# Kernel tuning notes

Measured on AMD Instinct MI355X. Metric: run time of the kernel, lower is better.

Reference implementation:

```python
import jax, jax.numpy as jnp
import numpy as np

B, C, Hf, Wf = 32, 512, 16, 16
S = Hf * Wf            # 256 kv tokens
D = 2048               # d_model
DIN = 512              # d_input (attention embed dim)
HEADS = 8
DH = DIN // HEADS
T = 50                 # iterations (internal ticks)
M = 25                 # memory_length
HH = 16                # memory_hidden_dims
NSA = 512              # n_synch_action
NSO = 512              # n_synch_out
OUT = 1000             # out_dims


def _ln(x, g, b, eps=1e-5):
    mu = x.mean(-1, keepdims=True)
    var = ((x - mu) ** 2).mean(-1, keepdims=True)
    return (x - mu) / jnp.sqrt(var + eps) * g + b


def _glu(x):
    a, b = jnp.split(x, 2, axis=-1)
    return a * jax.nn.sigmoid(b)


def setup_inputs() -> dict:
    key = jax.random.key(0)
    ki = iter(jax.random.split(key, 40))
    def rn(shape, s=0.02):
        return jax.random.normal(next(ki), shape, jnp.float32) * s
    inp = {}
    inp['x'] = jax.random.normal(next(ki), (B, C, Hf, Wf), jnp.float32)
    # kv_proj: Linear(C->DIN) + LayerNorm
    inp['kv_w'] = rn((C, DIN)); inp['kv_b'] = jnp.zeros((DIN,), jnp.float32)
    inp['ln_kv_g'] = jnp.ones((DIN,), jnp.float32); inp['ln_kv_b'] = jnp.zeros((DIN,), jnp.float32)
    # q_proj: Linear(NSA->DIN)
    inp['q_w'] = rn((NSA, DIN)); inp['q_b'] = jnp.zeros((DIN,), jnp.float32)
    # MultiheadAttention projections
    inp['Wq'] = rn((DIN, DIN)); inp['bq'] = jnp.zeros((DIN,), jnp.float32)
    inp['Wk'] = rn((DIN, DIN)); inp['bk'] = jnp.zeros((DIN,), jnp.float32)
    inp['Wv'] = rn((DIN, DIN)); inp['bv'] = jnp.zeros((DIN,), jnp.float32)
    inp['Wo'] = rn((DIN, DIN)); inp['bo'] = jnp.zeros((DIN,), jnp.float32)
    # synapse: Linear(DIN+D -> 2D) + GLU + LayerNorm(D)
    inp['syn_w'] = rn((DIN + D, 2 * D)); inp['syn_b'] = jnp.zeros((2 * D,), jnp.float32)
    inp['ln_syn_g'] = jnp.ones((D,), jnp.float32); inp['ln_syn_b'] = jnp.zeros((D,), jnp.float32)
    # per-neuron NLMs (SuperLinear weights: (in,out,N))
    inp['nlm_w1'] = rn((M, 2 * HH, D), 0.1); inp['nlm_b1'] = jnp.zeros((1, D, 2 * HH), jnp.float32)
    inp['nlm_w2'] = rn((HH, 2, D), 0.1); inp['nlm_b2'] = jnp.zeros((1, D, 2), jnp.float32)
    # output projector
    inp['out_w'] = rn((NSO, OUT)); inp['out_b'] = jnp.zeros((OUT,), jnp.float32)
    # learnable decay params (clamped to [0,15] in forward)
    inp['decay_action'] = jax.random.uniform(next(ki), (NSA,), jnp.float32)
    inp['decay_out'] = jax.random.uniform(next(ki), (NSO,), jnp.float32)
    # learned start state
    inp['start_trace'] = rn((D, M), 0.05)
    inp['start_act'] = rn((D,), 0.05)
    # random-pairing neuron indices (fixed at init in the original)
    inp['idx_la'] = jax.random.randint(next(ki), (NSA,), 0, D)
    inp['idx_ra'] = jax.random.randint(next(ki), (NSA,), 0, D)
    inp['idx_lo'] = jax.random.randint(next(ki), (NSO,), 0, D)
    inp['idx_ro'] = jax.random.randint(next(ki), (NSO,), 0, D)
    return inp


def reference(x, kv_w, kv_b, ln_kv_g, ln_kv_b, q_w, q_b, Wq, bq, Wk, bk, Wv, bv, Wo, bo,
              syn_w, syn_b, ln_syn_g, ln_syn_b, nlm_w1, nlm_b1, nlm_w2, nlm_b2,
              out_w, out_b, decay_action, decay_out, start_trace, start_act,
              idx_la, idx_ra, idx_lo, idx_ro):
    # featurise: identity backbone, flatten spatial to tokens, project to DIN
    feats = x.reshape(B, C, S).transpose(0, 2, 1)                 # (B,S,C)
    kv = _ln(feats @ kv_w + kv_b, ln_kv_g, ln_kv_b)               # (B,S,DIN)
    kh = (kv @ Wk + bk).reshape(B, S, HEADS, DH).transpose(0, 2, 1, 3)  # (B,H,S,DH)
    vh = (kv @ Wv + bv).reshape(B, S, HEADS, DH).transpose(0, 2, 1, 3)
    r_a = jnp.exp(-jnp.clip(decay_action, 0.0, 15.0))[None]       # (1,NSA)
    r_o = jnp.exp(-jnp.clip(decay_out, 0.0, 15.0))[None]          # (1,NSO)

    def nlm(trace):  # per-neuron MLP over the memory axis: (B,D,M) -> (B,D)
        h = _glu(jnp.einsum('bdm,mhd->bdh', trace, nlm_w1) + nlm_b1)
        return _glu(jnp.einsum('bdh,hod->bdo', h, nlm_w2) + nlm_b2)[..., 0]

    act0 = jnp.broadcast_to(start_act[None], (B, D))
    trace0 = jnp.broadcast_to(start_trace[None], (B, D, M))
    # out-synchronisation initialised from the start state (before the loop)
    a_o0 = act0[:, idx_lo] * act0[:, idx_ro]
    b_o0 = jnp.ones_like(a_o0)
    a_a0 = jnp.zeros((B, NSA), jnp.float32)
    b_a0 = jnp.zeros((B, NSA), jnp.float32)
    log_out = jnp.log(jnp.float32(OUT))
    scale = 1.0 / jnp.sqrt(jnp.float32(DH))

    def step(carry, _):
        trace, act, a_a, b_a, a_o, b_o = carry
        # action synchronisation (decayed pairwise products, sync = alpha/sqrt(beta))
        a_a = r_a * a_a + act[:, idx_la] * act[:, idx_ra]
        b_a = r_a * b_a + 1.0
        sync_a = a_a / jnp.sqrt(b_a)
        # attention readout (single query token)
        q = sync_a @ q_w + q_b                                    # (B,DIN)
        qh = (q @ Wq + bq).reshape(B, HEADS, 1, DH)
        attn = jax.nn.softmax(jnp.einsum('bhqd,bhkd->bhqk', qh, kh) * scale, -1)
        o = jnp.einsum('bhqk,bhkd->bhqd', attn, vh).transpose(0, 2, 1, 3).reshape(B, DIN)
        attn_out = o @ Wo + bo
        # synapse MLP -> new pre-activation state
        pre = jnp.concatenate([attn_out, act], axis=-1)           # (B,DIN+D)
        state = _ln(_glu(pre @ syn_w + syn_b), ln_syn_g, ln_syn_b)
        trace = jnp.concatenate([trace[:, :, 1:], state[:, :, None]], axis=-1)
        act = nlm(trace)                                          # (B,D)
        # output synchronisation + prediction
        a_o = r_o * a_o + act[:, idx_lo] * act[:, idx_ro]
        b_o = r_o * b_o + 1.0
        sync_o = a_o / jnp.sqrt(b_o)
        pred = sync_o @ out_w + out_b                             # (B,OUT)
        logp = jax.nn.log_softmax(pred, -1)
        ne = -(jnp.exp(logp) * logp).sum(-1) / log_out
        cert = jnp.stack([ne, 1.0 - ne], axis=-1)                 # (B,2)
        return (trace, act, a_a, b_a, a_o, b_o), (pred, cert, sync_o)

    _, (preds, certs, syncs) = jax.lax.scan(step, (trace0, act0, a_a0, b_a0, a_o0, b_o0), None, length=T)
    predictions = jnp.transpose(preds, (1, 2, 0))                 # (B,OUT,T)
    certainties = jnp.transpose(certs, (1, 2, 0))                 # (B,2,T)
    return predictions, certainties, syncs[-1]
```

## Files before the change

### kernel.cpp

```cpp
#include <hip/hip_runtime.h>
#include <math.h>

#define BB 32
#define CC 512
#define SS 256
#define DD 2048
#define DIN 512
#define NH 8
#define DHD 64
#define TT 50
#define MM 25
#define HHID 16
#define NSA 512
#define NSO 512
#define NOUT 1000

__global__ void init_kernel(const float* __restrict__ dec_a, const float* __restrict__ dec_o,
                            const float* __restrict__ start_act, const float* __restrict__ start_trace,
                            const int* __restrict__ idx_lo, const int* __restrict__ idx_ro,
                            float* __restrict__ r_a, float* __restrict__ r_o,
                            float* __restrict__ a_a, float* __restrict__ b_a,
                            float* __restrict__ a_o, float* __restrict__ b_o,
                            float* __restrict__ trace)
{
    int i = blockIdx.x * 256 + threadIdx.x;
    if (i < 512) {
        r_a[i] = expf(-fminf(fmaxf(dec_a[i], 0.f), 15.f));
        r_o[i] = expf(-fminf(fmaxf(dec_o[i], 0.f), 15.f));
    }
    if (i < BB * NSA) {
        a_a[i] = 0.f; b_a[i] = 0.f;
        int j = i & 511;
        a_o[i] = start_act[idx_lo[j]] * start_act[idx_ro[j]];
        b_o[i] = 1.f;
    }
    if (i < BB * MM * DD) {
        int rem = i % (MM * DD);
        int m = rem / DD, d = rem % DD;
        trace[i] = start_trace[d * MM + m];
    }
}

template<int AMODE, int SMODE>
__global__ void gemm64(const float* __restrict__ A, const float* __restrict__ Bm,
                       const float* __restrict__ bias, float* __restrict__ Cm,
                       int Mdim, int Ndim, int Kdim)
{
    __shared__ float As[16 * 65];
    __shared__ float Bs[16 * 64];
    int row0 = blockIdx.x * 64;
    int col0 = blockIdx.y * 64;
    int t = threadIdx.x;
    int tx = t & 15, ty = t >> 4;
    float acc[4][4] = {};
    for (int k0 = 0; k0 < Kdim; k0 += 16) {
        if (AMODE == 0) {
            for (int i = t; i < 1024; i += 256) {
                int kk = i & 15, r = i >> 4;
                As[kk * 65 + r] = A[(size_t)(row0 + r) * Kdim + k0 + kk];
            }
        } else {
            int b = row0 / SS, s0 = row0 % SS;
            for (int i = t; i < 1024; i += 256) {
                int r = i & 63, kk = i >> 6;
                As[kk * 65 + r] = A[((size_t)b * CC + k0 + kk) * SS + s0 + r];
            }
        }
        for (int i = t; i < 1024; i += 256) {
            int c = i & 63, kk = i >> 6;
            Bs[kk * 64 + c] = Bm[(size_t)(k0 + kk) * Ndim + col0 + c];
        }
        __syncthreads();
        #pragma unroll
        for (int kk = 0; kk < 16; ++kk) {
            float a[4], bb[4];
            #pragma unroll
            for (int i = 0; i < 4; i++) a[i] = As[kk * 65 + ty * 4 + i];
            #pragma unroll
            for (int j = 0; j < 4; j++) bb[j] = Bs[kk * 64 + tx * 4 + j];
            #pragma unroll
            for (int i = 0; i < 4; i++)
                #pragma unroll
                for (int j = 0; j < 4; j++) acc[i][j] += a[i] * bb[j];
        }
        __syncthreads();
    }
    #pragma unroll
    for (int i = 0; i < 4; i++)
        #pragma unroll
        for (int j = 0; j < 4; j++) {
            int row = row0 + ty * 4 + i, col = col0 + tx * 4 + j;
            float v = acc[i][j] + (bias ? bias[col] : 0.f);
            if (SMODE == 0) {
                Cm[(size_t)row * Ndim + col] = v;
            } else if (SMODE == 1) {
                int b = row / SS, s = row % SS, h = col >> 6, dh = col & 63;
                Cm[(((size_t)b * NH + h) * DHD + dh) * SS + s] = v;
            } else {
                int b = row / SS, s = row % SS, h = col >> 6, dh = col & 63;
                Cm[(((size_t)b * NH + h) * SS + s) * DHD + dh] = v;
            }
        }
}

__global__ void ln_rows(float* __restrict__ buf, const float* __restrict__ g,
                        const float* __restrict__ bta)
{
    int row = blockIdx.x, t = threadIdx.x;
    __shared__ float red[256];
    float v0 = buf[(size_t)row * 512 + t];
    float v1 = buf[(size_t)row * 512 + 256 + t];
    red[t] = v0 + v1; __syncthreads();
    for (int off = 128; off; off >>= 1) { if (t < off) red[t] += red[t + off]; __syncthreads(); }
    float mu = red[0] * (1.f / 512.f); __syncthreads();
    float d0 = v0 - mu, d1 = v1 - mu;
    red[t] = d0 * d0 + d1 * d1; __syncthreads();
    for (int off = 128; off; off >>= 1) { if (t < off) red[t] += red[t + off]; __syncthreads(); }
    float rstd = 1.f / sqrtf(red[0] * (1.f / 512.f) + 1e-5f);
    buf[(size_t)row * 512 + t]       = d0 * rstd * g[t] + bta[t];
    buf[(size_t)row * 512 + 256 + t] = d1 * rstd * g[t + 256] + bta[t + 256];
}

__global__ void bqq_kernel(const float* __restrict__ q_b, const float* __restrict__ Wq,
                           const float* __restrict__ bq, float* __restrict__ bqq)
{
    int c = blockIdx.x * 256 + threadIdx.x;
    if (c >= 512) return;
    float acc = bq[c];
    for (int k = 0; k < 512; k++) acc += q_b[k] * Wq[k * 512 + c];
    bqq[c] = acc;
}

__global__ void bias2_kernel(const float* __restrict__ bo, const float* __restrict__ syn_w,
                             const float* __restrict__ syn_b, float* __restrict__ bias2)
{
    int c = blockIdx.x * 256 + threadIdx.x;
    if (c >= 4096) return;
    float acc = syn_b[c];
    for (int k = 0; k < 512; k++) acc += bo[k] * syn_w[(size_t)k * 4096 + c];
    bias2[c] = acc;
}

__global__ void pad_act0(const float* __restrict__ out_w, const float* __restrict__ out_b,
                         const float* __restrict__ start_act,
                         float* __restrict__ out_wp, float* __restrict__ out_bp,
                         float* __restrict__ act0slot)
{
    int i = blockIdx.x * 256 + threadIdx.x;
    if (i < 512 * 1024) {
        int r = i >> 10, c = i & 1023;
        out_wp[i] = (c < 1000) ? out_w[r * 1000 + c] : 0.f;
    }
    if (i < 1024) out_bp[i] = (i < 1000) ? out_b[i] : 0.f;
    if (i < BB * DD) act0slot[i] = start_act[i & (DD - 1)];
}

__global__ __launch_bounds__(256) void k1_front(
    const float* __restrict__ act, const int* __restrict__ la, const int* __restrict__ ra,
    const float* __restrict__ r_a,
    const float* __restrict__ aold, const float* __restrict__ bold,
    float* __restrict__ anew, float* __restrict__ bnew,
    const float* __restrict__ Wqq, const float* __restrict__ bqq,
    const float* __restrict__ khT, const float* __restrict__ vh,
    float* __restrict__ obuf)
{
    __shared__ float sa[512];
    __shared__ float qp[256];
    __shared__ float qs[64];
    __shared__ float ps[256];
    __shared__ float red[256];
    int bh = blockIdx.x, b = bh >> 3, h = bh & 7;
    int tid = threadIdx.x;
    const float* actb = act + b * DD;
    for (int j = tid; j < 512; j += 256) {
        float p = actb[la[j]] * actb[ra[j]];
        float r = r_a[j];
        float aa = r * aold[b * 512 + j] + p;
        float bb = r * bold[b * 512 + j] + 1.f;
        sa[j] = aa / sqrtf(bb);
        if (h == 0) { anew[b * 512 + j] = aa; bnew[b * 512 + j] = bb; }
    }
    __syncthreads();
    {
        int cl = tid & 63, q = tid >> 6;
        const float* wcol = Wqq + h * 64 + cl;
        float acc = 0.f;
        #pragma unroll 8
        for (int k = q * 128; k < q * 128 + 128; ++k)
            acc += sa[k] * wcol[k * 512];
        qp[tid] = acc;
    }
    __syncthreads();
    if (tid < 64)
        qs[tid] = qp[tid] + qp[tid + 64] + qp[tid + 128] + qp[tid + 192] + bqq[h * 64 + tid];
    __syncthreads();
    const float* kb = khT + (size_t)bh * 64 * 256;
    float sc = 0.f;
    #pragma unroll 8
    for (int dh = 0; dh < 64; ++dh) sc += qs[dh] * kb[dh * 256 + tid];
    sc *= 0.125f;
    red[tid] = sc; __syncthreads();
    for (int off = 128; off; off >>= 1) { if (tid < off) red[tid] = fmaxf(red[tid], red[tid + off]); __syncthreads(); }
    float mx = red[0]; __syncthreads();
    float e = expf(sc - mx);
    red[tid] = e; __syncthreads();
    for (int off = 128; off; off >>= 1) { if (tid < off) red[tid] += red[tid + off]; __syncthreads(); }
    float inv = 1.f / red[0];
    ps[tid] = e * inv;
    __syncthreads();
    int dh = tid & 63, ch = tid >> 6;
    const float* vb = vh + (size_t)bh * 256 * 64;
    float acc = 0.f;
    for (int s = ch * 64; s < ch * 64 + 64; ++s) acc += ps[s] * vb[s * 64 + dh];
    red[tid] = acc; __syncthreads();
    if (tid < 128) red[tid] += red[tid + 128];
    __syncthreads();
    if (tid < 64) obuf[b * 512 + h * 64 + tid] = red[tid] + red[tid + 64];
}

#define SYN_PAD 164
__global__ __launch_bounds__(256) void k2_syn(
    const float* __restrict__ obuf, const float* __restrict__ act,
    const float* __restrict__ W2, const float* __restrict__ syn_w,
    float* __restrict__ upart)
{
    __shared__ float As[32 * SYN_PAD];
    int tid = threadIdx.x;
    int ks = blockIdx.x & 3, ct = blockIdx.x >> 2;
    int cgr = tid & 7, r = tid >> 3;
    int c = ct * 32 + cgr * 4;
    int kbase0 = ks * 640;
    float acc0 = 0.f, acc1 = 0.f, acc2 = 0.f, acc3 = 0.f;
    for (int ri = 0; ri < 4; ++ri) {
        __syncthreads();
        #pragma unroll
        for (int q = 0; q < 5; ++q) {
            int i = tid + q * 256;
            int rr = i / 40, kg = i % 40;
            int k = kbase0 + ri * 160 + kg * 4;
            float4 v;
            if (k < 512) v = *(const float4*)(obuf + rr * 512 + k);
            else         v = *(const float4*)(act + rr * 2048 + (k - 512));
            *(float4*)(As + rr * SYN_PAD + kg * 4) = v;
        }
        __syncthreads();
        const float* Ar = As + r * SYN_PAD;
        int kbase = kbase0 + ri * 160;
        for (int kk = 0; kk < 160; kk += 8) {
            float4 wreg[8];
            #pragma unroll
            for (int u8 = 0; u8 < 8; ++u8) {
                int kg = kbase + kk + u8;
                const float* wr = (kg < 512 ? W2 : syn_w) + (size_t)kg * 4096 + c;
                wreg[u8] = *(const float4*)wr;
            }
            #pragma unroll
            for (int u8 = 0; u8 < 8; ++u8) {
                float a = Ar[kk + u8];
                acc0 += a * wreg[u8].x; acc1 += a * wreg[u8].y;
                acc2 += a * wreg[u8].z; acc3 += a * wreg[u8].w;
            }
        }
    }
    *(float4*)(upart + (size_t)ks * (32 * 4096) + r * 4096 + c) =
        make_float4(acc0, acc1, acc2, acc3);
}

__global__ __launch_bounds__(256) void k34_glunlm(
    const float* __restrict__ upart, const float* __restrict__ bias2,
    const float* __restrict__ g, const float* __restrict__ bta,
    float* __restrict__ trace,
    const float* __restrict__ w1, const float* __restrict__ b1,
    const float* __restrict__ w2, const float* __restrict__ b2,
    float* __restrict__ actout, int t_iter)
{
    __shared__ float red[256];
    int blk = blockIdx.x, tid = threadIdx.x;
    int b = blk >> 3, dtile = blk & 7;
    const float* u0 = upart + (size_t)b * 4096;
    float vals[8];
    float loc = 0.f;
    #pragma unroll
    for (int ii = 0; ii < 8; ++ii) {
        int d = tid + ii * 256;
        float a = bias2[d], bb = bias2[d + 2048];
        #pragma unroll
        for (int ks = 0; ks < 4; ++ks) {
            const float* up = u0 + (size_t)ks * (32 * 4096);
            a += up[d];
            bb += up[d + 2048];
        }
        float gl = a * (1.f / (1.f + expf(-bb)));
        vals[ii] = gl; loc += gl;
    }
    red[tid] = loc; __syncthreads();
    for (int off = 128; off; off >>= 1) { if (tid < off) red[tid] += red[tid + off]; __syncthreads(); }
    float mu = red[0] * (1.f / 2048.f); __syncthreads();
    float l2 = 0.f;
    #pragma unroll
    for (int ii = 0; ii < 8; ++ii) { float dq = vals[ii] - mu; l2 += dq * dq; }
    red[tid] = l2; __syncthreads();
    for (int off = 128; off; off >>= 1) { if (tid < off) red[tid] += red[tid + off]; __syncthreads(); }
    float rstd = 1.f / sqrtf(red[0] * (1.f / 2048.f) + 1e-5f);
    int d0 = dtile * 256 + tid;
    float a0 = bias2[d0], bb0 = bias2[d0 + 2048];
    #pragma unroll
    for (int ks = 0; ks < 4; ++ks) {
        const float* up = u0 + (size_t)ks * (32 * 4096);
        a0 += up[d0];
        bb0 += up[d0 + 2048];
    }
    float gl0 = a0 * (1.f / (1.f + expf(-bb0)));
    float nv = (gl0 - mu) * rstd * g[d0] + bta[d0];
    int newrow = t_iter % MM;
    trace[((size_t)b * MM + newrow) * DD + d0] = nv;
    float hp[32];
    #pragma unroll
    for (int h = 0; h < 32; h++) hp[h] = b1[d0 * 32 + h];
    const float* tr = trace + (size_t)b * MM * DD;
    for (int m = 0; m < 24; m++) {
        int mph = (t_iter + 1 + m) % 25;
        float tv = tr[mph * DD + d0];
        #pragma unroll
        for (int h = 0; h < 32; h++) hp[h] += tv * w1[((size_t)m * 32 + h) * DD + d0];
    }
    #pragma unroll
    for (int h = 0; h < 32; h++) hp[h] += nv * w1[((size_t)24 * 32 + h) * DD + d0];
    float o0 = b2[d0 * 2], o1 = b2[d0 * 2 + 1];
    #pragma unroll
    for (int h = 0; h < 16; h++) {
        float hv = hp[h] * (1.f / (1.f + expf(-hp[h + 16])));
        o0 += hv * w2[((size_t)h * 2) * DD + d0];
        o1 += hv * w2[((size_t)h * 2 + 1) * DD + d0];
    }
    actout[b * DD + d0] = o0 * (1.f / (1.f + expf(-o1)));
}

__global__ __launch_bounds__(256) void k_syncscan(
    const float* __restrict__ acthist, const int* __restrict__ lo, const int* __restrict__ ro,
    const float* __restrict__ r_o,
    const float* __restrict__ a_o0, const float* __restrict__ b_o0,
    float* __restrict__ so_hist, float* __restrict__ out_sync)
{
    int idx = blockIdx.x * 256 + threadIdx.x;
    int b = idx >> 9, j = idx & 511;
    float aa = a_o0[idx], bb = b_o0[idx];
    float rr = r_o[j];
    int il = lo[j], ir = ro[j];
    const float* ah = acthist + (size_t)(BB * DD) + b * DD;
    float s = 0.f;
    for (int t = 0; t < TT; ++t) {
        float p = ah[il] * ah[ir];
        aa = rr * aa + p;
        bb = rr * bb + 1.f;
        s = aa / sqrtf(bb);
        so_hist[(size_t)t * (BB * 512) + idx] = s;
        ah += BB * DD;
    }
    out_sync[idx] = s;
}

__global__ __launch_bounds__(256) void k6_cert(
    const float* __restrict__ predt, float* __restrict__ d_out)
{
    int t_iter = blockIdx.x >> 5, b = blockIdx.x & 31, t = threadIdx.x;
    __shared__ float red[256];
    const float* pr = predt + ((size_t)t_iter * 32 + b) * 1024;
    float pv[4];
    float mx = -1e30f;
    #pragma unroll
    for (int ii = 0; ii < 4; ++ii) {
        int c = t + ii * 256;
        float v = -1e30f;
        if (c < 1000) {
            v = pr[c];
            d_out[(size_t)b * NOUT * TT + (size_t)c * TT + t_iter] = v;
        }
        pv[ii] = v;
        mx = fmaxf(mx, v);
    }
    red[t] = mx; __syncthreads();
    for (int off = 128; off; off >>= 1) { if (t < off) red[t] = fmaxf(red[t], red[t + off]); __syncthreads(); }
    mx = red[0]; __syncthreads();
    float s1 = 0.f, s2 = 0.f;
    #pragma unroll
    for (int ii = 0; ii < 4; ++ii) {
        int c = t + ii * 256;
        if (c < 1000) { float xx = pv[ii] - mx; float e = expf(xx); s1 += e; s2 += e * xx; }
    }
    red[t] = s1; __syncthreads();
    for (int off = 128; off; off >>= 1) { if (t < off) red[t] += red[t + off]; __syncthreads(); }
    s1 = red[0]; __syncthreads();
    red[t] = s2; __syncthreads();
    for (int off = 128; off; off >>= 1) { if (t < off) red[t] += red[t + off]; __syncthreads(); }
    s2 = red[0];
    if (t == 0) {
        float ne = -(s2 / s1 - logf(s1)) * (1.f / logf(1000.f));
        size_t base = (size_t)BB * NOUT * TT + (size_t)b * 2 * TT + t_iter;
        d_out[base] = ne;
        d_out[base + TT] = 1.f - ne;
    }
}

extern "C" void kernel_launch(void* const* d_in, const int* in_sizes, int n_in,
                              void* d_out, int out_size, void* d_ws, size_t ws_size,
                              hipStream_t stream)
{
    const float* x        = (const float*)d_in[0];
    const float* kv_w     = (const float*)d_in[1];
    const float* kv_b     = (const float*)d_in[2];
    const float* ln_kv_g  = (const float*)d_in[3];
    const float* ln_kv_b  = (const float*)d_in[4];
    const float* q_w      = (const float*)d_in[5];
    const float* q_b      = (const float*)d_in[6];
    const float* Wq       = (const float*)d_in[7];
    const float* bq       = (const float*)d_in[8];
    const float* Wk       = (const float*)d_in[9];
    const float* bk       = (const float*)d_in[10];
    const float* Wv       = (const float*)d_in[11];
    const float* bv       = (const float*)d_in[12];
    const float* Wo       = (const float*)d_in[13];
    const float* bo       = (const float*)d_in[14];
    const float* syn_w    = (const float*)d_in[15];
    const float* syn_b    = (const float*)d_in[16];
    const float* ln_syn_g = (const float*)d_in[17];
    const float* ln_syn_b = (const float*)d_in[18];
    const float* nlm_w1   = (const float*)d_in[19];
    const float* nlm_b1   = (const float*)d_in[20];
    const float* nlm_w2   = (const float*)d_in[21];
    const float* nlm_b2   = (const float*)d_in[22];
    const float* out_w    = (const float*)d_in[23];
    const float* out_b    = (const float*)d_in[24];
    const float* dec_a    = (const float*)d_in[25];
    const float* dec_o    = (const float*)d_in[26];
    const float* start_tr = (const float*)d_in[27];
    const float* start_ac = (const float*)d_in[28];
    const int*   idx_la   = (const int*)d_in[29];
    const int*   idx_ra   = (const int*)d_in[30];
    const int*   idx_lo   = (const int*)d_in[31];
    const int*   idx_ro   = (const int*)d_in[32];
    float* out = (float*)d_out;

    float* w = (float*)d_ws;
    float* kvbuf = w;            w += (size_t)8192 * 512;
    float* khT   = w;            w += (size_t)8192 * 512;
    float* vhb   = w;            w += (size_t)8192 * 512;
    float* Wqq   = w;            w += (size_t)512 * 512;
    float* bqq   = w;            w += 512;
    float* W2    = w;            w += (size_t)512 * 4096;
    float* bias2 = w;            w += 4096;
    float* r_a   = w;            w += 512;
    float* r_o   = w;            w += 512;
    float* a_a   = w;            w += 2 * BB * NSA;
    float* b_a   = w;            w += 2 * BB * NSA;
    float* a_o   = w;            w += BB * NSO;
    float* b_o   = w;            w += BB * NSO;
    float* trace = w;            w += (size_t)BB * MM * DD;
    float* obuf  = w;            w += BB * DIN;
    float* upart = w;            w += (size_t)4 * 32 * 4096;
    float* so_hist = w;          w += (size_t)TT * BB * 512;
    float* predt = w;            w += (size_t)TT * BB * 1024;
    float* out_wp = w;           w += (size_t)512 * 1024;
    float* out_bp = w;           w += 1024;

    float* acthist = kvbuf;

    init_kernel<<<6400, 256, 0, stream>>>(dec_a, dec_o, start_ac, start_tr, idx_lo, idx_ro,
                                          r_a, r_o, a_a, b_a, a_o, b_o, trace);
    gemm64<1, 0><<<dim3(128, 8), 256, 0, stream>>>(x, kv_w, kv_b, kvbuf, 8192, 512, 512);
    ln_rows<<<8192, 256, 0, stream>>>(kvbuf, ln_kv_g, ln_kv_b);
    gemm64<0, 1><<<dim3(128, 8), 256, 0, stream>>>(kvbuf, Wk, bk, khT, 8192, 512, 512);
    gemm64<0, 2><<<dim3(128, 8), 256, 0, stream>>>(kvbuf, Wv, bv, vhb, 8192, 512, 512);
    gemm64<0, 0><<<dim3(8, 8), 256, 0, stream>>>(q_w, Wq, nullptr, Wqq, 512, 512, 512);
    bqq_kernel<<<2, 256, 0, stream>>>(q_b, Wq, bq, bqq);
    gemm64<0, 0><<<dim3(8, 64), 256, 0, stream>>>(Wo, syn_w, nullptr, W2, 512, 4096, 512);
    bias2_kernel<<<16, 256, 0, stream>>>(bo, syn_w, syn_b, bias2);
    pad_act0<<<2048, 256, 0, stream>>>(out_w, out_b, start_ac, out_wp, out_bp, acthist);

    float* out_sync = out + (size_t)BB * NOUT * TT + (size_t)BB * 2 * TT;

    for (int t = 0; t < TT; ++t) {
        int par = t & 1;
        const float* act_t = acthist + (size_t)t * (BB * DD);
        float* act_n = acthist + (size_t)(t + 1) * (BB * DD);
        k1_front<<<256, 256, 0, stream>>>(act_t, idx_la, idx_ra, r_a,
                                          a_a + par * (BB * 512), b_a + par * (BB * 512),
                                          a_a + (par ^ 1) * (BB * 512), b_a + (par ^ 1) * (BB * 512),
                                          Wqq, bqq, khT, vhb, obuf);
        k2_syn<<<512, 256, 0, stream>>>(obuf, act_t, W2, syn_w, upart);
        k34_glunlm<<<256, 256, 0, stream>>>(upart, bias2, ln_syn_g, ln_syn_b, trace,
                                            nlm_w1, nlm_b1, nlm_w2, nlm_b2, act_n, t);
    }

    k_syncscan<<<64, 256, 0, stream>>>(acthist, idx_lo, idx_ro, r_o, a_o, b_o,
                                       so_hist, out_sync);
    gemm64<0, 0><<<dim3(25, 16), 256, 0, stream>>>(so_hist, out_wp, out_bp, predt,
                                                   1600, 1024, 512);
    k6_cert<<<1600, 256, 0, stream>>>(predt, out);
}
```

Before: 5.209 ms.

## Fuse synapse GEMM with GLU and LN partial stats, stage NLM weights in LDS

Pre-transposes the combined synapse weight into a k-contiguous WT layout. The per-step synapse GEMM now computes both GLU halves per output column over the full K, with no split-K. The kernel applies GLU in place and emits per-batch sum and sum-of-squares partials, which removes the upart round trip and the LayerNorm re-reduction. The NLM kernel is retiled to 8 batches × 32 neurons and stages its w1 slice (about 100KB) in dynamic LDS. Variance is now computed as E[x^2]-mu^2, which is less numerically stable. The large LDS use limits occupancy, and each block in the GEMM kernel covers only 8 columns with per-thread strided weight reads.

Result: slower. 5.901 ms (+13.3%).

```diff
diff --git a/kernel.cpp b/kernel.cpp
--- a/kernel.cpp
+++ b/kernel.cpp
@@ -141,10 +141,36 @@
     bias2[c] = acc;
 }
 
-__global__ void pad_act0(const float* __restrict__ out_w, const float* __restrict__ out_b,
-                         const float* __restrict__ start_act,
-                         float* __restrict__ out_wp, float* __restrict__ out_bp,
-                         float* __restrict__ act0slot)
+__global__ void wt_build(const float* __restrict__ W2, const float* __restrict__ syn_w,
+                         float* __restrict__ WT)
+{
+    __shared__ float tile[32][33];
+    int k0 = blockIdx.x * 32, c0 = blockIdx.y * 32;
+    int t = threadIdx.x;
+    int col = t & 31, rq = t >> 5;
+    #pragma unroll
+    for (int q = 0; q < 4; ++q) {
+        int kk = q * 8 + rq;
+        int k = k0 + kk;
+        const float* src = (k < 512 ? W2 : syn_w) + (size_t)k * 4096 + c0;
+        tile[kk][col] = src[col];
+    }
+    __syncthreads();
+    #pragma unroll
+    for (int q = 0; q < 4; ++q) {
+        int cc = q * 8 + rq;
+        WT[(size_t)(c0 + cc) * 2560 + k0 + col] = tile[col][cc];
+    }
+}
+
+__global__ void act0_kernel(const float* __restrict__ start_act, float* __restrict__ act0slot)
+{
+    int i = blockIdx.x * 256 + threadIdx.x;
+    if (i < BB * DD) act0slot[i] = start_act[i & (DD - 1)];
+}
+
+__global__ void pad_outw(const float* __restrict__ out_w, const float* __restrict__ out_b,
+                         float* __restrict__ out_wp, float* __restrict__ out_bp)
 {
     int i = blockIdx.x * 256 + threadIdx.x;
     if (i < 512 * 1024) {
@@ -152,7 +178,6 @@
         out_wp[i] = (c < 1000) ? out_w[r * 1000 + c] : 0.f;
     }
     if (i < 1024) out_bp[i] = (i < 1000) ? out_b[i] : 0.f;
-    if (i < BB * DD) act0slot[i] = start_act[i & (DD - 1)];
 }
 
 __global__ __launch_bounds__(256) void k1_front(
@@ -218,122 +243,142 @@
     if (tid < 64) obuf[b * 512 + h * 64 + tid] = red[tid] + red[tid + 64];
 }
 
-#define SYN_PAD 164
-__global__ __launch_bounds__(256) void k2_syn(
+__global__ __launch_bounds__(256) void k2_glu(
     const float* __restrict__ obuf, const float* __restrict__ act,
-    const float* __restrict__ W2, const float* __restrict__ syn_w,
-    float* __restrict__ upart)
-{
-    __shared__ float As[32 * SYN_PAD];
-    int tid = threadIdx.x;
-    int ks = blockIdx.x & 3, ct = blockIdx.x >> 2;
-    int cgr = tid & 7, r = tid >> 3;
-    int c = ct * 32 + cgr * 4;
-    int kbase0 = ks * 640;
-    float acc0 = 0.f, acc1 = 0.f, acc2 = 0.f, acc3 = 0.f;
-    for (int ri = 0; ri < 4; ++ri) {
+    const float* __restrict__ WT, const float* __restrict__ bias2,
+    float* __restrict__ glbufT, float* __restrict__ partials)
+{
+    __shared__ float As[32 * 160];
+    int tid = threadIdx.x, blk = blockIdx.x;
+    int cpair = tid >> 5, r = tid & 31;
+    int c = blk * 8 + cpair;
+    const float* wta = WT + (size_t)c * 2560;
+    const float* wtb = WT + (size_t)(c + 2048) * 2560;
+    float acc_a = 0.f, acc_b = 0.f;
+    for (int ri = 0; ri < 16; ++ri) {
         __syncthreads();
         #pragma unroll
         for (int q = 0; q < 5; ++q) {
             int i = tid + q * 256;
             int rr = i / 40, kg = i % 40;
-            int k = kbase0 + ri * 160 + kg * 4;
+            int k = ri * 160 + kg * 4;
             float4 v;
             if (k < 512) v = *(const float4*)(obuf + rr * 512 + k);
             else         v = *(const float4*)(act + rr * 2048 + (k - 512));
-            *(float4*)(As + rr * SYN_PAD + kg * 4) = v;
+            *(float4*)(As + rr * 160 + ((kg ^ (rr & 7)) << 2)) = v;
         }
         __syncthreads();
-        const float* Ar = As + r * SYN_PAD;
-        int kbase = kbase0 + ri * 160;
-        for (int kk = 0; kk < 160; kk += 8) {
-            float4 wreg[8];
-            #pragma unroll
-            for (int u8 = 0; u8 < 8; ++u8) {
-                int kg = kbase + kk + u8;
-                const float* wr = (kg < 512 ? W2 : syn_w) + (size_t)kg * 4096 + c;
-                wreg[u8] = *(const float4*)wr;
-            }
-            #pragma unroll
-            for (int u8 = 0; u8 < 8; ++u8) {
-                float a = Ar[kk + u8];
-                acc0 += a * wreg[u8].x; acc1 += a * wreg[u8].y;
-                acc2 += a * wreg[u8].z; acc3 += a * wreg[u8].w;
-            }
-        }
-    }
-    *(float4*)(upart + (size_t)ks * (32 * 4096) + r * 4096 + c) =
-        make_float4(acc0, acc1, acc2, acc3);
-}
-
-__global__ __launch_bounds__(256) void k34_glunlm(
-    const float* __restrict__ upart, const float* __restrict__ bias2,
+        int kbase = ri * 160;
+        const float* Ar = As + r * 160;
+        int sw = r & 7;
+        #pragma unroll 8
+        for (int kc = 0; kc < 40; ++kc) {
+            float4 a4 = *(const float4*)(Ar + ((kc ^ sw) << 2));
+            float4 wa = *(const float4*)(wta + kbase + kc * 4);
+            float4 wb = *(const float4*)(wtb + kbase + kc * 4);
+            acc_a += a4.x * wa.x + a4.y * wa.y + a4.z * wa.z + a4.w * wa.w;
+            acc_b += a4.x * wb.x + a4.y * wb.y + a4.z * wb.z + a4.w * wb.w;
+        }
+    }
+    float ua = acc_a + bias2[c];
+    float ub = acc_b + bias2[c + 2048];
+    float gl = ua * (1.f / (1.f + expf(-ub)));
+    glbufT[c * 32 + r] = gl;
+    __syncthreads();
+    float* ps1 = As;
+    float* ps2 = As + 256;
+    ps1[tid] = gl;
+    ps2[tid] = gl * gl;
+    __syncthreads();
+    if (tid < 32) {
+        float s = 0.f, s2 = 0.f;
+        #pragma unroll
+        for (int cp = 0; cp < 8; ++cp) { s += ps1[cp * 32 + tid]; s2 += ps2[cp * 32 + tid]; }
+        partials[blk * 64 + tid * 2]     = s;
+        partials[blk * 64 + tid * 2 + 1] = s2;
+    }
+}
+
+#define K4_LDS_FLOATS (25600 + 256 + 256 + 16)
+__global__ __launch_bounds__(256) void k4_nlm(
+    const float* __restrict__ glbufT, const float* __restrict__ partials,
     const float* __restrict__ g, const float* __restrict__ bta,
     float* __restrict__ trace,
     const float* __restrict__ w1, const float* __restrict__ b1,
     const float* __restrict__ w2, const float* __restrict__ b2,
     float* __restrict__ actout, int t_iter)
 {
-    __shared__ float red[256];
-    int blk = blockIdx.x, tid = threadIdx.x;
-    int b = blk >> 3, dtile = blk & 7;
-    const float* u0 = upart + (size_t)b * 4096;
-    float vals[8];
-    float loc = 0.f;
-    #pragma unroll
-    for (int ii = 0; ii < 8; ++ii) {
-        int d = tid + ii * 256;
-        float a = bias2[d], bb = bias2[d + 2048];
-        #pragma unroll
-        for (int ks = 0; ks < 4; ++ks) {
-            const float* up = u0 + (size_t)ks * (32 * 4096);
-            a += up[d];
-            bb += up[d + 2048];
-        }
-        float gl = a * (1.f / (1.f + expf(-bb)));
-        vals[ii] = gl; loc += gl;
-    }
-    red[tid] = loc; __syncthreads();
-    for (int off = 128; off; off >>= 1) { if (tid < off) red[tid] += red[tid + off]; __syncthreads(); }
-    float mu = red[0] * (1.f / 2048.f); __syncthreads();
-    float l2 = 0.f;
-    #pragma unroll
-    for (int ii = 0; ii < 8; ++ii) { float dq = vals[ii] - mu; l2 += dq * dq; }
-    red[tid] = l2; __syncthreads();
-    for (int off = 128; off; off >>= 1) { if (tid < off) red[tid] += red[tid + off]; __syncthreads(); }
-    float rstd = 1.f / sqrtf(red[0] * (1.f / 2048.f) + 1e-5f);
-    int d0 = dtile * 256 + tid;
-    float a0 = bias2[d0], bb0 = bias2[d0 + 2048];
-    #pragma unroll
-    for (int ks = 0; ks < 4; ++ks) {
-        const float* up = u0 + (size_t)ks * (32 * 4096);
-        a0 += up[d0];
-        bb0 += up[d0 + 2048];
-    }
-    float gl0 = a0 * (1.f / (1.f + expf(-bb0)));
-    float nv = (gl0 - mu) * rstd * g[d0] + bta[d0];
+    extern __shared__ float lds[];
+    float* wlds = lds;
+    float* r1 = lds + 25600;
+    float* r2 = lds + 25856;
+    float* sm = lds + 26112;
+    int tid = threadIdx.x, blk = blockIdx.x;
+    int dtile = blk & 63, bgrp = blk >> 6;
+    int d0 = dtile * 32, b0 = bgrp * 8;
+    int b_l = tid >> 5, d_l = tid & 31;
+    int b = b0 + b_l, d = d0 + d_l;
+
+    for (int q = 0; q < 100; ++q) {
+        int i = tid + q * 256;
+        wlds[i] = w1[(size_t)(i >> 5) * 2048 + d0 + (i & 31)];
+    }
+    {
+        int j = tid & 31;
+        float s = 0.f, s2 = 0.f;
+        #pragma unroll
+        for (int q = 0; q < 8; ++q) {
+            int kblk = j + 32 * q;
+            s  += partials[kblk * 64 + b * 2];
+            s2 += partials[kblk * 64 + b * 2 + 1];
+        }
+        r1[tid] = s; r2[tid] = s2;
+        __syncthreads();
+        for (int off = 16; off; off >>= 1) {
+            if (j < off) { r1[tid] += r1[tid + off]; r2[tid] += r2[tid + off]; }
+            __syncthreads();
+        }
+        if (j == 0) {
+            float mu = r1[tid] * (1.f / 2048.f);
+            float var = r2[tid] * (1.f / 2048.f) - mu * mu;
+            sm[b_l * 2] = mu;
+            sm[b_l * 2 + 1] = 1.f / sqrtf(var + 1e-5f);
+        }
+        __syncthreads();
+    }
+    float mu = sm[b_l * 2], rstd = sm[b_l * 2 + 1];
+    float gl = glbufT[d * 32 + b];
+    float nv = (gl - mu) * rstd * g[d] + bta[d];
     int newrow = t_iter % MM;
-    trace[((size_t)b * MM + newrow) * DD + d0] = nv;
+    trace[((size_t)b * MM + newrow) * DD + d] = nv;
+
     float hp[32];
-    #pragma unroll
-    for (int h = 0; h < 32; h++) hp[h] = b1[d0 * 32 + h];
-    const float* tr = trace + (size_t)b * MM * DD;
+    {
+        const float* b1d = b1 + d * 32;
+        #pragma unroll
+        for (int h = 0; h < 32; h++) hp[h] = b1d[h];
+    }
+    const float* trb = trace + (size_t)b * MM * DD + d;
     for (int m = 0; m < 24; m++) {
         int mph = (t_iter + 1 + m) % 25;
-        float tv = tr[mph * DD + d0];
-        #pragma unroll
-        for (int h = 0; h < 32; h++) hp[h] += tv * w1[((size_t)m * 32 + h) * DD + d0];
-    }
-    #pragma unroll
-    for (int h = 0; h < 32; h++) hp[h] += nv * w1[((size_t)24 * 32 + h) * DD + d0];
-    float o0 = b2[d0 * 2], o1 = b2[d0 * 2 + 1];
+        float tv = trb[(size_t)mph * DD];
+        const float* wm = wlds + m * 1024 + d_l;
+        #pragma unroll
+        for (int h = 0; h < 32; h++) hp[h] += tv * wm[h * 32];
+    }
+    {
+        const float* wm = wlds + 24 * 1024 + d_l;
+        #pragma unroll
+        for (int h = 0; h < 32; h++) hp[h] += nv * wm[h * 32];
+    }
+    float o0 = b2[d * 2], o1 = b2[d * 2 + 1];
     #pragma unroll
     for (int h = 0; h < 16; h++) {
         float hv = hp[h] * (1.f / (1.f + expf(-hp[h + 16])));
-        o0 += hv * w2[((size_t)h * 2) * DD + d0];
-        o1 += hv * w2[((size_t)h * 2 + 1) * DD + d0];
-    }
-    actout[b * DD + d0] = o0 * (1.f / (1.f + expf(-o1)));
+        o0 += hv * w2[((size_t)h * 2) * DD + d];
+        o1 += hv * w2[((size_t)h * 2 + 1) * DD + d];
+    }
+    actout[b * DD + d] = o0 * (1.f / (1.f + expf(-o1)));
 }
 
 __global__ __launch_bounds__(256) void k_syncscan(
@@ -448,6 +493,7 @@
     float* Wqq   = w;            w += (size_t)512 * 512;
     float* bqq   = w;            w += 512;
     float* W2    = w;            w += (size_t)512 * 4096;
+    float* WT    = w;            w += (size_t)4096 * 2560;
     float* bias2 = w;            w += 4096;
     float* r_a   = w;            w += 512;
     float* r_o   = w;            w += 512;
@@ -457,13 +503,14 @@
     float* b_o   = w;            w += BB * NSO;
     float* trace = w;            w += (size_t)BB * MM * DD;
     float* obuf  = w;            w += BB * DIN;
-    float* upart = w;            w += (size_t)4 * 32 * 4096;
-    float* so_hist = w;          w += (size_t)TT * BB * 512;
-    float* predt = w;            w += (size_t)TT * BB * 1024;
-    float* out_wp = w;           w += (size_t)512 * 1024;
-    float* out_bp = w;           w += 1024;
+    float* glbufT = w;           w += (size_t)DD * BB;
+    float* partials = w;         w += 256 * 32 * 2;
 
     float* acthist = kvbuf;
+    float* so_hist = vhb;
+    float* out_wp  = khT;
+    float* out_bp  = khT + 524288;
+    float* predt   = W2;
 
     init_kernel<<<6400, 256, 0, stream>>>(dec_a, dec_o, start_ac, start_tr, idx_lo, idx_ro,
                                           r_a, r_o, a_a, b_a, a_o, b_o, trace);
@@ -475,9 +522,18 @@
     bqq_kernel<<<2, 256, 0, stream>>>(q_b, Wq, bq, bqq);
     gemm64<0, 0><<<dim3(8, 64), 256, 0, stream>>>(Wo, syn_w, nullptr, W2, 512, 4096, 512);
     bias2_kernel<<<16, 256, 0, stream>>>(bo, syn_w, syn_b, bias2);
-    pad_act0<<<2048, 256, 0, stream>>>(out_w, out_b, start_ac, out_wp, out_bp, acthist);
+    wt_build<<<dim3(80, 128), 256, 0, stream>>>(W2, syn_w, WT);
+    act0_kernel<<<256, 256, 0, stream>>>(start_ac, acthist);
 
     float* out_sync = out + (size_t)BB * NOUT * TT + (size_t)BB * 2 * TT;
+
+    static int lds_attr_set = 0;
+    if (!lds_attr_set) {
+        hipFuncSetAttribute(reinterpret_cast<const void*>(k4_nlm),
+                            hipFuncAttributeMaxDynamicSharedMemorySize,
+                            K4_LDS_FLOATS * 4);
+        lds_attr_set = 1;
+    }
 
     for (int t = 0; t < TT; ++t) {
         int par = t & 1;
@@ -487,13 +543,15 @@
                                           a_a + par * (BB * 512), b_a + par * (BB * 512),
                                           a_a + (par ^ 1) * (BB * 512), b_a + (par ^ 1) * (BB * 512),
                                           Wqq, bqq, khT, vhb, obuf);
-        k2_syn<<<512, 256, 0, stream>>>(obuf, act_t, W2, syn_w, upart);
-        k34_glunlm<<<256, 256, 0, stream>>>(upart, bias2, ln_syn_g, ln_syn_b, trace,
+        k2_glu<<<256, 256, 0, stream>>>(obuf, act_t, WT, bias2, glbufT, partials);
+        k4_nlm<<<256, 256, K4_LDS_FLOATS * 4, stream>>>(glbufT, partials,
+                                            ln_syn_g, ln_syn_b, trace,
                                             nlm_w1, nlm_b1, nlm_w2, nlm_b2, act_n, t);
     }
 
     k_syncscan<<<64, 256, 0, stream>>>(acthist, idx_lo, idx_ro, r_o, a_o, b_o,
                                        so_hist, out_sync);
+    pad_outw<<<2048, 256, 0, stream>>>(out_w, out_b, out_wp, out_bp);
     gemm64<0, 0><<<dim3(25, 16), 256, 0, stream>>>(so_hist, out_wp, out_bp, predt,
                                                    1600, 1024, 512);
     k6_cert<<<1600, 256, 0, stream>>>(predt, out);
```
